# Kernel tuning notes

Measured on AMD Instinct MI355X. Metric: run time of the kernel, lower is better.

Reference implementation:

```python
import jax, jax.numpy as jnp
import numpy as np

OUT_FEATURES = 4096
IN_FEATURES = 4096
GROUP_SIZE = 128
NUM_GROUPS = IN_FEATURES // GROUP_SIZE  # 32
PACKED_SIZE = OUT_FEATURES * IN_FEATURES // 8  # 2097152


def setup_inputs() -> dict:
    key = jax.random.key(0)
    k1, k2, k3, k4 = jax.random.split(key, 4)
    x = jax.random.normal(k1, (2, 512, IN_FEATURES), dtype=jnp.float32)
    # random packed 4-bit weights (8 nibbles per int32)
    w_packed = jax.random.randint(k2, (PACKED_SIZE,), jnp.iinfo(jnp.int32).min,
                                  jnp.iinfo(jnp.int32).max, dtype=jnp.int32)
    w_scale = jax.random.uniform(k3, (OUT_FEATURES, NUM_GROUPS), dtype=jnp.float32) * 0.05
    w_zero = jax.random.randint(k4, (OUT_FEATURES, NUM_GROUPS), 0, 8, dtype=jnp.int32)
    return {"x": x, "w_packed": w_packed, "w_scale": w_scale, "w_zero": w_zero}


def _unpack_dequant(w_packed, w_scale, w_zero):
    # Extract 8 nibbles per int32: (v >> (i*4)) & 0xF, i = 0..7
    shifts = jnp.arange(8, dtype=jnp.int32) * 4
    nibbles = (w_packed[:, None] >> shifts[None, :]) & 15  # [packed, 8]
    w4 = nibbles.reshape(-1)  # [out*in], values 0..15
    w4 = jnp.where(w4 >= 8, w4 - 16, w4)  # signed 4-bit -> [-8, 7]
    w_int = w4.reshape(OUT_FEATURES, NUM_GROUPS, GROUP_SIZE).astype(jnp.float32)
    # per-(row, group) dequant: (q - zero) * scale
    w = (w_int - w_zero[:, :, None].astype(jnp.float32)) * w_scale[:, :, None]
    return w.reshape(OUT_FEATURES, IN_FEATURES)


def reference(x, w_packed, w_scale, w_zero):
    weight = _unpack_dequant(w_packed, w_scale, w_zero).astype(x.dtype)
    # F.linear: y = x @ W^T
    return jnp.einsum('bsi,oi->bso', x, weight)
```

## Files before the change

kernel.cpp:

```cpp
#include <hip/hip_runtime.h>
#include <hip/hip_bf16.h>
#include <stdint.h>

#define IN_F 4096
#define OUT_F 4096
#define NG 32

typedef __attribute__((ext_vector_type(8))) short short8;
typedef __attribute__((ext_vector_type(4))) float floatx4;

__global__ __launch_bounds__(256) void dequant_kernel(
    const int* __restrict__ wp, const float* __restrict__ scale,
    const int* __restrict__ zero, __hip_bfloat16* __restrict__ Wb) {
  int p = blockIdx.x * 256 + threadIdx.x;
  int row = p >> 9;
  int g = (p >> 4) & 31;
  float s = scale[row * NG + g];
  float zs = (float)zero[row * NG + g] * s;
  unsigned v = (unsigned)wp[p];
  union { __hip_bfloat16 h[8]; uint4 u4; } o;
#pragma unroll
  for (int i = 0; i < 8; ++i) {
    int q = (int)((v >> (4 * i)) & 15u);
    q -= (q >= 8) ? 16 : 0;
    o.h[i] = __float2bfloat16((float)q * s - zs);
  }
  *(uint4*)(Wb + (size_t)p * 8) = o.u4;
}

__global__ __launch_bounds__(256) void convert_kernel(
    const float* __restrict__ x, __hip_bfloat16* __restrict__ xb) {
  int i = blockIdx.x * 256 + threadIdx.x;
  float4 v = ((const float4*)x)[i];
  union { __hip_bfloat16 h[4]; uint2 u; } o;
  o.h[0] = __float2bfloat16(v.x);
  o.h[1] = __float2bfloat16(v.y);
  o.h[2] = __float2bfloat16(v.z);
  o.h[3] = __float2bfloat16(v.w);
  ((uint2*)xb)[i] = o.u;
}

#define BM 128
#define BN 128
#define BK 64
#define SPLITK 2

__global__ __launch_bounds__(256) void gemm_bt(
    const __hip_bfloat16* __restrict__ A, const __hip_bfloat16* __restrict__ Bt,
    float* __restrict__ C0, float* __restrict__ C1, int M, int N, int K) {
  __shared__ short Alds[BM * BK];
  __shared__ short Blds[BN * BK];

  int t = threadIdx.x;
  int wave = t >> 6, lane = t & 63;
  int wm = (wave >> 1) * 64, wn = (wave & 1) * 64;
  int r = lane & 15, quad = lane >> 4;
  int bm = blockIdx.y * BM, bn = blockIdx.x * BN;
  int kz = blockIdx.z * (K / SPLITK);
  int kend = kz + K / SPLITK;

  floatx4 acc[4][4] = {};

  const __hip_bfloat16* Ag = A + (size_t)bm * K;
  const __hip_bfloat16* Bg = Bt + (size_t)bn * K;

  for (int k0 = kz; k0 < kend; k0 += BK) {
    __syncthreads();
#pragma unroll
    for (int j = 0; j < 4; ++j) {
      int c = t + 256 * j;
      int row = c >> 3, kc = c & 7;
      const __hip_bfloat16* ga = Ag + (size_t)row * K + k0 + kc * 8;
      const __hip_bfloat16* gb = Bg + (size_t)row * K + k0 + kc * 8;
      __builtin_amdgcn_global_load_lds(
          (const __attribute__((address_space(1))) void*)ga,
          (__attribute__((address_space(3))) void*)(&Alds[c * 8]), 16, 0, 0);
      __builtin_amdgcn_global_load_lds(
          (const __attribute__((address_space(1))) void*)gb,
          (__attribute__((address_space(3))) void*)(&Blds[c * 8]), 16, 0, 0);
    }
    __syncthreads();

#pragma unroll
    for (int ks = 0; ks < 2; ++ks) {
      int kk = ks * 32;
      short8 af[4], bf[4];
#pragma unroll
      for (int mi = 0; mi < 4; ++mi)
        af[mi] = *(const short8*)&Alds[(wm + mi * 16 + r) * BK + kk + quad * 8];
#pragma unroll
      for (int ni = 0; ni < 4; ++ni)
        bf[ni] = *(const short8*)&Blds[(wn + ni * 16 + r) * BK + kk + quad * 8];
#pragma unroll
      for (int mi = 0; mi < 4; ++mi)
#pragma unroll
        for (int ni = 0; ni < 4; ++ni)
          acc[mi][ni] = __builtin_amdgcn_mfma_f32_16x16x32_bf16(
              af[mi], bf[ni], acc[mi][ni], 0, 0, 0);
    }
  }

  float* C = (blockIdx.z == 0) ? C0 : C1;
#pragma unroll
  for (int mi = 0; mi < 4; ++mi) {
#pragma unroll
    for (int ni = 0; ni < 4; ++ni) {
#pragma unroll
      for (int i = 0; i < 4; ++i) {
        int grow = bm + wm + mi * 16 + quad * 4 + i;
        int gcol = bn + wn + ni * 16 + r;
        C[(size_t)grow * N + gcol] = acc[mi][ni][i];
      }
    }
  }
}

__global__ __launch_bounds__(256) void reduce_kernel(
    float* __restrict__ out, const float* __restrict__ part) {
  int i = blockIdx.x * 256 + threadIdx.x;
  float4 a = ((const float4*)out)[i];
  float4 b = ((const float4*)part)[i];
  a.x += b.x; a.y += b.y; a.z += b.z; a.w += b.w;
  ((float4*)out)[i] = a;
}

extern "C" void kernel_launch(void* const* d_in, const int* in_sizes, int n_in,
                              void* d_out, int out_size, void* d_ws, size_t ws_size,
                              hipStream_t stream) {
  const float* x = (const float*)d_in[0];
  const int* wp = (const int*)d_in[1];
  const float* wscale = (const float*)d_in[2];
  const int* wzero = (const int*)d_in[3];
  float* out = (float*)d_out;

  int M = in_sizes[0] / IN_F;

  __hip_bfloat16* Wb = (__hip_bfloat16*)d_ws;
  __hip_bfloat16* Xb = (__hip_bfloat16*)((char*)d_ws + (size_t)OUT_F * IN_F * 2);
  float* Cpart = (float*)((char*)d_ws + (size_t)OUT_F * IN_F * 2 + (size_t)M * IN_F * 2);

  dequant_kernel<<<(OUT_F * IN_F / 8) / 256, 256, 0, stream>>>(wp, wscale, wzero, Wb);
  convert_kernel<<<(M * IN_F / 4) / 256, 256, 0, stream>>>(x, Xb);

  dim3 grid(OUT_F / BN, M / BM, SPLITK);
  gemm_bt<<<grid, 256, 0, stream>>>(Xb, Wb, out, Cpart, M, OUT_F, IN_F);

  reduce_kernel<<<(M * OUT_F / 4) / 256, 256, 0, stream>>>(out, Cpart);
}
```

Measured before the change: 138.4 us.

## Fuse int4 dequantization into GEMM B-tile load using fp16 magic-number unpacking

Drops the standalone dequant kernel that wrote a full bf16 weight matrix to workspace. The GEMM now loads packed int4 words directly, dequantizes them in registers with a 0x6400 fp16 magic-bias trick and precomputed packed scale/zero pairs, and writes the result into LDS. Activations are converted to fp16 in a matching pair-interleaved k order, and the MFMA switches from bf16 to f16. The N tile shrinks to 64 and occupancy is hinted at 4 blocks per CU. This removes the large weight write/read traffic, at the cost of some fp16 rounding of x (round-toward-zero) and extra ALU work inside the GEMM loop.

```diff
diff --git a/kernel.cpp b/kernel.cpp
--- a/kernel.cpp
+++ b/kernel.cpp
@@ -1,101 +1,128 @@
 #include <hip/hip_runtime.h>
-#include <hip/hip_bf16.h>
 #include <stdint.h>
 
 #define IN_F 4096
 #define OUT_F 4096
 #define NG 32
 
-typedef __attribute__((ext_vector_type(8))) short short8;
+typedef __attribute__((ext_vector_type(8))) _Float16 half8;
+typedef __attribute__((ext_vector_type(2))) _Float16 half2t;
 typedef __attribute__((ext_vector_type(4))) float floatx4;
 
-__global__ __launch_bounds__(256) void dequant_kernel(
-    const int* __restrict__ wp, const float* __restrict__ scale,
-    const int* __restrict__ zero, __hip_bfloat16* __restrict__ Wb) {
-  int p = blockIdx.x * 256 + threadIdx.x;
-  int row = p >> 9;
-  int g = (p >> 4) & 31;
-  float s = scale[row * NG + g];
-  float zs = (float)zero[row * NG + g] * s;
-  unsigned v = (unsigned)wp[p];
-  union { __hip_bfloat16 h[8]; uint4 u4; } o;
-#pragma unroll
-  for (int i = 0; i < 8; ++i) {
-    int q = (int)((v >> (4 * i)) & 15u);
-    q -= (q >= 8) ? 16 : 0;
-    o.h[i] = __float2bfloat16((float)q * s - zs);
+__global__ __launch_bounds__(256) void prep_kernel(
+    const float* __restrict__ x, _Float16* __restrict__ Xh,
+    const float* __restrict__ wscale, const int* __restrict__ wzero,
+    uint2* __restrict__ SZ, int nxb) {
+  int b = blockIdx.x;
+  if (b < nxb) {
+    int i = b * 256 + threadIdx.x;
+    const float4* x4 = (const float4*)x;
+    float4 a = x4[2 * i];
+    float4 c = x4[2 * i + 1];
+    uint4 o;
+    o.x = __builtin_bit_cast(unsigned, __builtin_amdgcn_cvt_pkrtz(a.x, c.x));
+    o.y = __builtin_bit_cast(unsigned, __builtin_amdgcn_cvt_pkrtz(a.y, c.y));
+    o.z = __builtin_bit_cast(unsigned, __builtin_amdgcn_cvt_pkrtz(a.z, c.z));
+    o.w = __builtin_bit_cast(unsigned, __builtin_amdgcn_cvt_pkrtz(a.w, c.w));
+    ((uint4*)Xh)[i] = o;
+  } else {
+    int i = (b - nxb) * 256 + threadIdx.x;
+    float s = wscale[i];
+    int zp = wzero[i];
+    _Float16 sh = (_Float16)s;
+    _Float16 ch = (_Float16)(float)(1032 + zp);
+    unsigned s2 = (unsigned)__builtin_bit_cast(unsigned short, sh) * 0x10001u;
+    unsigned c2 = (unsigned)__builtin_bit_cast(unsigned short, ch) * 0x10001u;
+    SZ[i] = make_uint2(s2, c2);
   }
-  *(uint4*)(Wb + (size_t)p * 8) = o.u4;
-}
-
-__global__ __launch_bounds__(256) void convert_kernel(
-    const float* __restrict__ x, __hip_bfloat16* __restrict__ xb) {
-  int i = blockIdx.x * 256 + threadIdx.x;
-  float4 v = ((const float4*)x)[i];
-  union { __hip_bfloat16 h[4]; uint2 u; } o;
-  o.h[0] = __float2bfloat16(v.x);
-  o.h[1] = __float2bfloat16(v.y);
-  o.h[2] = __float2bfloat16(v.z);
-  o.h[3] = __float2bfloat16(v.w);
-  ((uint2*)xb)[i] = o.u;
 }
 
 #define BM 128
-#define BN 128
+#define BN 64
 #define BK 64
 #define SPLITK 2
 
-__global__ __launch_bounds__(256) void gemm_bt(
-    const __hip_bfloat16* __restrict__ A, const __hip_bfloat16* __restrict__ Bt,
+__device__ __forceinline__ uint4 dequant8(unsigned v, uint2 szv) {
+  unsigned tx = v ^ 0x88888888u;
+  half2t s2 = __builtin_bit_cast(half2t, szv.x);
+  half2t c2 = __builtin_bit_cast(half2t, szv.y);
+  unsigned p0 = (tx & 0x000F000Fu) | 0x64006400u;
+  unsigned p1 = ((tx >> 4) & 0x000F000Fu) | 0x64006400u;
+  unsigned p2 = ((tx >> 8) & 0x000F000Fu) | 0x64006400u;
+  unsigned p3 = ((tx >> 12) & 0x000F000Fu) | 0x64006400u;
+  half2t w0 = (__builtin_bit_cast(half2t, p0) - c2) * s2;
+  half2t w1 = (__builtin_bit_cast(half2t, p1) - c2) * s2;
+  half2t w2 = (__builtin_bit_cast(half2t, p2) - c2) * s2;
+  half2t w3 = (__builtin_bit_cast(half2t, p3) - c2) * s2;
+  uint4 o;
+  o.x = __builtin_bit_cast(unsigned, w0);
+  o.y = __builtin_bit_cast(unsigned, w1);
+  o.z = __builtin_bit_cast(unsigned, w2);
+  o.w = __builtin_bit_cast(unsigned, w3);
+  return o;
+}
+
+__global__ __launch_bounds__(256, 4) void gemm_fused(
+    const _Float16* __restrict__ A, const int* __restrict__ wp,
+    const uint2* __restrict__ SZ,
     float* __restrict__ C0, float* __restrict__ C1, int M, int N, int K) {
-  __shared__ short Alds[BM * BK];
-  __shared__ short Blds[BN * BK];
+  __shared__ _Float16 Alds[BM * BK];
+  __shared__ _Float16 Blds[BN * BK];
 
   int t = threadIdx.x;
   int wave = t >> 6, lane = t & 63;
-  int wm = (wave >> 1) * 64, wn = (wave & 1) * 64;
+  int wm = (wave >> 1) * 64, wn = (wave & 1) * 32;
   int r = lane & 15, quad = lane >> 4;
   int bm = blockIdx.y * BM, bn = blockIdx.x * BN;
   int kz = blockIdx.z * (K / SPLITK);
   int kend = kz + K / SPLITK;
 
-  floatx4 acc[4][4] = {};
+  floatx4 acc[4][2] = {};
 
-  const __hip_bfloat16* Ag = A + (size_t)bm * K;
-  const __hip_bfloat16* Bg = Bt + (size_t)bn * K;
+  const _Float16* Ag = A + (size_t)bm * K;
+  int rowb = t >> 3, m8 = t & 7;
+  const int* wpr0 = wp + (size_t)(bn + rowb) * (IN_F / 8) + m8;
+  const int* wpr1 = wp + (size_t)(bn + rowb + 32) * (IN_F / 8) + m8;
+  const uint2* sz0 = SZ + (size_t)(bn + rowb) * NG;
+  const uint2* sz1 = SZ + (size_t)(bn + rowb + 32) * NG;
 
   for (int k0 = kz; k0 < kend; k0 += BK) {
+    unsigned v0 = (unsigned)wpr0[k0 >> 3];
+    unsigned v1 = (unsigned)wpr1[k0 >> 3];
+    uint2 szv0 = sz0[k0 >> 7];
+    uint2 szv1 = sz1[k0 >> 7];
+
     __syncthreads();
+
 #pragma unroll
     for (int j = 0; j < 4; ++j) {
       int c = t + 256 * j;
       int row = c >> 3, kc = c & 7;
-      const __hip_bfloat16* ga = Ag + (size_t)row * K + k0 + kc * 8;
-      const __hip_bfloat16* gb = Bg + (size_t)row * K + k0 + kc * 8;
+      const _Float16* ga = Ag + (size_t)row * K + k0 + kc * 8;
       __builtin_amdgcn_global_load_lds(
           (const __attribute__((address_space(1))) void*)ga,
           (__attribute__((address_space(3))) void*)(&Alds[c * 8]), 16, 0, 0);
-      __builtin_amdgcn_global_load_lds(
-          (const __attribute__((address_space(1))) void*)gb,
-          (__attribute__((address_space(3))) void*)(&Blds[c * 8]), 16, 0, 0);
     }
+    ((uint4*)Blds)[t] = dequant8(v0, szv0);
+    ((uint4*)Blds)[t + 256] = dequant8(v1, szv1);
+
     __syncthreads();
 
 #pragma unroll
     for (int ks = 0; ks < 2; ++ks) {
       int kk = ks * 32;
-      short8 af[4], bf[4];
+      half8 af[4], bf[2];
 #pragma unroll
       for (int mi = 0; mi < 4; ++mi)
-        af[mi] = *(const short8*)&Alds[(wm + mi * 16 + r) * BK + kk + quad * 8];
+        af[mi] = *(const half8*)&Alds[(wm + mi * 16 + r) * BK + kk + quad * 8];
 #pragma unroll
-      for (int ni = 0; ni < 4; ++ni)
-        bf[ni] = *(const short8*)&Blds[(wn + ni * 16 + r) * BK + kk + quad * 8];
+      for (int ni = 0; ni < 2; ++ni)
+        bf[ni] = *(const half8*)&Blds[(wn + ni * 16 + r) * BK + kk + quad * 8];
 #pragma unroll
       for (int mi = 0; mi < 4; ++mi)
 #pragma unroll
-        for (int ni = 0; ni < 4; ++ni)
-          acc[mi][ni] = __builtin_amdgcn_mfma_f32_16x16x32_bf16(
+        for (int ni = 0; ni < 2; ++ni)
+          acc[mi][ni] = __builtin_amdgcn_mfma_f32_16x16x32_f16(
               af[mi], bf[ni], acc[mi][ni], 0, 0, 0);
     }
   }
@@ -104,7 +131,7 @@
 #pragma unroll
   for (int mi = 0; mi < 4; ++mi) {
 #pragma unroll
-    for (int ni = 0; ni < 4; ++ni) {
+    for (int ni = 0; ni < 2; ++ni) {
 #pragma unroll
       for (int i = 0; i < 4; ++i) {
         int grow = bm + wm + mi * 16 + quad * 4 + i;
@@ -135,15 +162,16 @@
 
   int M = in_sizes[0] / IN_F;
 
-  __hip_bfloat16* Wb = (__hip_bfloat16*)d_ws;
-  __hip_bfloat16* Xb = (__hip_bfloat16*)((char*)d_ws + (size_t)OUT_F * IN_F * 2);
-  float* Cpart = (float*)((char*)d_ws + (size_t)OUT_F * IN_F * 2 + (size_t)M * IN_F * 2);
+  _Float16* Xh = (_Float16*)d_ws;
+  float* Cpart = (float*)((char*)d_ws + (size_t)M * IN_F * 2);
+  uint2* SZ = (uint2*)((char*)d_ws + (size_t)M * IN_F * 2 + (size_t)M * OUT_F * 4);
 
-  dequant_kernel<<<(OUT_F * IN_F / 8) / 256, 256, 0, stream>>>(wp, wscale, wzero, Wb);
-  convert_kernel<<<(M * IN_F / 4) / 256, 256, 0, stream>>>(x, Xb);
+  int nxb = (M * IN_F / 8) / 256;
+  int nzb = (OUT_F * NG) / 256;
+  prep_kernel<<<nxb + nzb, 256, 0, stream>>>(x, Xh, wscale, wzero, SZ, nxb);
 
   dim3 grid(OUT_F / BN, M / BM, SPLITK);
-  gemm_bt<<<grid, 256, 0, stream>>>(Xb, Wb, out, Cpart, M, OUT_F, IN_F);
+  gemm_fused<<<grid, 256, 0, stream>>>(Xh, wp, SZ, out, Cpart, M, OUT_F, IN_F);
 
   reduce_kernel<<<(M * OUT_F / 4) / 256, 256, 0, stream>>>(out, Cpart);
 }
```

New measurement: 146.4 us. 1.06x slower.
